# Optimization experiments

Measured on AMD Instinct MI355X. Metric: run time of the kernel, lower is better.

## Reference

```python
import jax, jax.numpy as jnp
import numpy as np

B, S, D, H = 2, 4096, 128, 128
EPS = 1e-6
NEG_INF = -1e30


def _complex_linear(xr, xi, Wr, Wi, br, bi):
    # x: (B,S,D); W: (H,D); complex linear (Wr + i Wi)(xr + i xi) + (br + i bi) per layer math:
    # real_out = (xr Wr + br) - (xi Wi + bi); imag_out = (xi Wr + br) + (xr Wi + bi)
    out_r = xr @ Wr.T + br - (xi @ Wi.T + bi)
    out_i = xi @ Wr.T + br + (xr @ Wi.T + bi)
    return out_r, out_i


def setup_inputs() -> dict:
    key = jax.random.key(0)
    ks = jax.random.split(key, 24)
    scale = 1.0 / np.sqrt(D)
    def W(k):
        return jax.random.normal(k, (H, D), jnp.float32) * scale
    def b(k):
        return jax.random.normal(k, (H,), jnp.float32) * 0.01
    inp = {
        "Z_q": jax.random.normal(ks[0], (B, 2, S, D, 1), jnp.float32),
        "Z_k": jax.random.normal(ks[1], (B, 2, S, D, 1), jnp.float32),
        "Z_v": jax.random.normal(ks[2], (B, 2, S, D, 1), jnp.float32),
        "Wq_r": W(ks[3]), "Wq_i": W(ks[4]), "bq_r": b(ks[5]), "bq_i": b(ks[6]),
        "Wk_r": W(ks[7]), "Wk_i": W(ks[8]), "bk_r": b(ks[9]), "bk_i": b(ks[10]),
        "Wv_r": W(ks[11]), "Wv_i": W(ks[12]), "bv_r": b(ks[13]), "bv_i": b(ks[14]),
        "Wp_r": W(ks[15]), "Wp_i": W(ks[16]), "bp_r": b(ks[17]), "bp_i": b(ks[18]),
        "noise_floor": jnp.asarray(1.0, jnp.float32),
        "tau": jnp.asarray(0.0, jnp.float32),
    }
    return inp


def reference(Z_q, Z_k, Z_v,
              Wq_r, Wq_i, bq_r, bq_i,
              Wk_r, Wk_i, bk_r, bk_i,
              Wv_r, Wv_i, bv_r, bv_i,
              Wp_r, Wp_i, bp_r, bp_i,
              noise_floor, tau):
    # squeeze trailing singleton; split real/imag -> (B,S,D)
    zqr, zqi = Z_q[:, 0, :, :, 0], Z_q[:, 1, :, :, 0]
    zkr, zki = Z_k[:, 0, :, :, 0], Z_k[:, 1, :, :, 0]
    zvr, zvi = Z_v[:, 0, :, :, 0], Z_v[:, 1, :, :, 0]

    Qr, Qi = _complex_linear(zqr, zqi, Wq_r, Wq_i, bq_r, bq_i)
    Kr, Ki = _complex_linear(zkr, zki, Wk_r, Wk_i, bk_r, bk_i)
    Vr, Vi = _complex_linear(zvr, zvi, Wv_r, Wv_i, bv_r, bv_i)

    # InverseMahalanobis: R2[b,i,j] = sum_h |Q[b,i]-K[b,j]|^2
    q2 = jnp.sum(Qr * Qr + Qi * Qi, axis=-1)          # (B,S)
    k2 = jnp.sum(Kr * Kr + Ki * Ki, axis=-1)          # (B,S)
    re_qk = (jnp.einsum('bsh,bth->bst', Qr, Kr)
             + jnp.einsum('bsh,bth->bst', Qi, Ki))    # (B,S,S)
    R2 = q2[:, :, None] + k2[:, None, :] - 2.0 * re_qk

    attn_scores = -jax.nn.softplus(tau) * jnp.log(noise_floor ** 2 + R2 + EPS)
    mask = jnp.tril(jnp.ones((S, S), dtype=bool))[None]
    attn_scores = jnp.where(mask, attn_scores, NEG_INF)
    attn_weights = jax.nn.softmax(attn_scores / jnp.sqrt(jnp.float32(H)), axis=-1)

    # attn (real) times complex V
    est_r = jnp.einsum('bst,bth->bsh', attn_weights, Vr)
    est_i = jnp.einsum('bst,bth->bsh', attn_weights, Vi)

    out_r, out_i = _complex_linear(est_r, est_i, Wp_r, Wp_i, bp_r, bp_i)
    out = jnp.stack((out_r, out_i), axis=1)[..., None]  # (B,2,S,H,1)
    return out, attn_weights
```

## Files before the change

### kernel.cpp

```cpp
#include <hip/hip_runtime.h>

#define S_LEN 4096
#define NBATCH 2
#define ROWS (NBATCH*S_LEN)
#define OUT_ELEMS 2097152

typedef _Float16 f16;
typedef _Float16 f16x8 __attribute__((ext_vector_type(8)));
typedef _Float16 f16x4 __attribute__((ext_vector_type(4)));
typedef float f32x4 __attribute__((ext_vector_type(4)));

#define MT_OFF    0x000000
#define BIAS_OFF  0x080000
#define SC_OFF    0x081000
#define QH_OFF    0x100000
#define KH_OFF    0x500000
#define VT_OFF    0x900000
#define Q2_OFF    0xD00000
#define K2_OFF    0xD10000
#define L_OFF     0xD20000
#define EST_OFF   0xE00000
#define PW_OFF    0x1600000
#define WS_NEED   0x5600000

#define MFMA16(A,B,C) __builtin_amdgcn_mfma_f32_16x16x32_f16(A,B,C,0,0,0)

__device__ __forceinline__ void async_cp16(f16* lds, const f16* g) {
  __builtin_amdgcn_global_load_lds(
      (const __attribute__((address_space(1))) void*)g,
      (__attribute__((address_space(3))) void*)lds, 16, 0, 0);
}

__device__ __forceinline__ void stage16(f16* lds, const f16* g, int stride, int tid) {
#pragma unroll
  for (int i = 0; i < 2; ++i) {
    int idx = i*256 + tid;
    int row = idx >> 2, c = idx & 3;
    async_cp16(lds + idx*8, g + (size_t)row*stride + c*8);
  }
}

__device__ __forceinline__ void stage32(f16* lds, const float* g, int stride, int tid,
                                        const float* rowscale) {
#pragma unroll
  for (int i = 0; i < 4; ++i) {
    int idx = i*256 + tid;
    int row = idx >> 3, c = idx & 7;
    const float4* gp = (const float4*)(g + (size_t)row*stride + c*4);
    float4 v = *gp;
    float sc = rowscale ? rowscale[row] : 1.0f;
    f16x4 h; h[0]=(f16)(v.x*sc); h[1]=(f16)(v.y*sc); h[2]=(f16)(v.z*sc); h[3]=(f16)(v.w*sc);
    *(f16x4*)(lds + row*32 + c*4) = h;
  }
}

__device__ __forceinline__ void mfma_step(const f16* Asm, const f16* Bsm, int lane,
                                          int wm, int wn, f32x4 acc[4][4]) {
  f16x8 a[4], b[4];
  int rr = lane & 15, kk = (lane >> 4) << 3;
#pragma unroll
  for (int i=0;i<4;i++) a[i] = *(const f16x8*)(Asm + (wm + i*16 + rr)*32 + kk);
#pragma unroll
  for (int j=0;j<4;j++) b[j] = *(const f16x8*)(Bsm + (wn + j*16 + rr)*32 + kk);
#pragma unroll
  for (int i=0;i<4;i++)
#pragma unroll
    for (int j=0;j<4;j++) acc[i][j] = MFMA16(a[i], b[j], acc[i][j]);
}

__global__ __launch_bounds__(256)
void k_build(const float* Wqr, const float* Wqi, const float* bqr, const float* bqi,
             const float* Wkr, const float* Wki, const float* bkr, const float* bki,
             const float* Wvr, const float* Wvi, const float* bvr, const float* bvi,
             const float* Wpr, const float* Wpi, const float* bpr, const float* bpi,
             f16* Mt, float* bias) {
  int mat = blockIdx.x;
  const float *Wr, *Wi, *br, *bi;
  if (mat == 0)      { Wr=Wqr; Wi=Wqi; br=bqr; bi=bqi; }
  else if (mat == 1) { Wr=Wkr; Wi=Wki; br=bkr; bi=bki; }
  else if (mat == 2) { Wr=Wvr; Wi=Wvi; br=bvr; bi=bvi; }
  else               { Wr=Wpr; Wi=Wpi; br=bpr; bi=bpi; }
  int idx = blockIdx.y*256 + threadIdx.x;
  int n = idx >> 8, k = idx & 255;
  int d = k & 127, h = n & 127;
  float w = (k < 128) ? ((n < 128) ? Wr[h*128+d] : Wi[h*128+d])
                      : ((n < 128) ? -Wi[h*128+d] : Wr[h*128+d]);
  Mt[mat*65536 + n*256 + k] = (f16)w;
  if (k == 0)
    bias[mat*256 + n] = (n < 128) ? (br[n] - bi[n]) : (br[n-128] + bi[n-128]);
}

__global__ __launch_bounds__(256)
void k_init(float* est, float* zreg, float* sc, const float* nf, const float* tau) {
  int idx = blockIdx.x*256 + threadIdx.x;
  if (idx < 524288) ((float4*)est)[idx] = make_float4(0.f,0.f,0.f,0.f);
  else { int j = idx - 524288; if (j < 12288) ((float4*)zreg)[j] = make_float4(0.f,0.f,0.f,0.f); }
  if (idx == 0) {
    float t = tau[0];
    float c = __builtin_log2f(1.0f + __builtin_exp2f(t * 1.4426950408889634f))
              * 0.6931471805599453f;
    sc[0] = -c * 0.08838834764831845f;
    sc[1] = nf[0]*nf[0] + 1e-6f;
  }
}

__global__ __launch_bounds__(256)
void k_proj(const float* Zq, const float* Zk, const float* Zv,
            const f16* Mt, const float* bias,
            f16* Qh, f16* Kh, f16* Vt, float* q2, float* k2) {
  __shared__ f16 Asm[128*32];
  __shared__ f16 Bsm[128*32];
  __shared__ float bias_s[128];
  int tid = threadIdx.x;
  int mode = blockIdx.z;
  int m0 = blockIdx.x * 128, n0 = blockIdx.y * 128;
  const float* Z = (mode==0) ? Zq : (mode==1 ? Zk : Zv);
  const f16* Bt = Mt + mode*65536;
  if (tid < 128) bias_s[tid] = bias[mode*256 + n0 + tid];
  int b = m0 >> 12, s0 = m0 & 4095;
  int lane = tid & 63, w = tid >> 6;
  int wm = (w >> 1)*64, wn = (w & 1)*64;
  f32x4 acc[4][4] = {};
  for (int kb = 0; kb < 8; ++kb) {
    int k0 = kb*32;
    int part = k0 >> 7, d0 = k0 & 127;
    const float* Ag = Z + (((size_t)(b*2 + part))*S_LEN + s0)*128 + d0;
    stage32(Asm, Ag, 128, tid, nullptr);
    stage16(Bsm, Bt + n0*256 + k0, 256, tid);
    __syncthreads();
    mfma_step(Asm, Bsm, lane, wm, wn, acc);
    __syncthreads();
  }
  int rr = (lane>>4)*4, cc = lane & 15;
  if (mode < 2) {
    f16* O = (mode==0) ? Qh : Kh;
    float rs[4][4];
#pragma unroll
    for (int i=0;i<4;i++)
#pragma unroll
      for (int r=0;r<4;r++) rs[i][r]=0.f;
#pragma unroll
    for (int i=0;i<4;i++)
#pragma unroll
      for (int j=0;j<4;j++) {
        int cl = wn + j*16 + cc;
        int cg = n0 + cl;
        float bv = bias_s[cl];
#pragma unroll
        for (int r=0;r<4;r++) {
          int rg = m0 + wm + i*16 + rr + r;
          f16 hv = (f16)(acc[i][j][r] + bv);
          O[(size_t)rg*256 + cg] = hv;
          float fv = (float)hv;
          rs[i][r] += fv*fv;
        }
      }
#pragma unroll
    for (int m=8;m>=1;m>>=1)
#pragma unroll
      for (int i=0;i<4;i++)
#pragma unroll
        for (int r=0;r<4;r++) rs[i][r] += __shfl_xor(rs[i][r], m, 64);
    if (cc == 0) {
      float* T = (mode==0) ? q2 : k2;
#pragma unroll
      for (int i=0;i<4;i++)
#pragma unroll
        for (int r=0;r<4;r++) {
          int rg = m0 + wm + i*16 + rr + r;
          atomicAdd(&T[rg], rs[i][r]);
        }
    }
  } else {
#pragma unroll
    for (int i=0;i<4;i++) {
      int t0 = s0 + wm + i*16 + rr;
#pragma unroll
      for (int j=0;j<4;j++) {
        int cl = wn + j*16 + cc;
        int cg = n0 + cl;
        float bv = bias_s[cl];
        f16x4 h4;
#pragma unroll
        for (int r=0;r<4;r++) h4[r] = (f16)(acc[i][j][r] + bv);
        *(f16x4*)(Vt + (size_t)b*1048576 + (size_t)cg*4096 + t0) = h4;
      }
    }
  }
}

__global__ __launch_bounds__(256)
void k_attn(const f16* Qh, const f16* Kh, const float* q2, const float* k2,
            const float* sc, float* lsum, f16* Pws, float* attn) {
  int x = blockIdx.x;
  int b = x >> 10, r = x & 1023;
  int sb = r >> 5, tb = r & 31;
  int s0 = sb*128, t0 = tb*128;
  int tid = threadIdx.x;
  if (tb > sb) {
    float4 z = make_float4(0.f,0.f,0.f,0.f);
    int row = tid >> 1, h = tid & 1;
    float4* p = (float4*)(attn + ((size_t)(b*S_LEN) + s0 + row)*S_LEN + t0 + h*64);
#pragma unroll
    for (int i=0;i<16;i++) p[i] = z;
    return;
  }
  __shared__ f16 Asm[128*32];
  __shared__ f16 Bsm[128*32];
  __shared__ float q2s[128], k2s[128];
  if (tid < 128) {
    q2s[tid] = q2[b*S_LEN + s0 + tid];
    k2s[tid] = k2[b*S_LEN + t0 + tid];
  }
  float kc = sc[0], nf2 = sc[1];
  int lane = tid & 63, w = tid >> 6;
  int wm = (w >> 1)*64, wn = (w & 1)*64;
  const f16* Ag = Qh + ((size_t)(b*S_LEN) + s0)*256;
  const f16* Bg = Kh + ((size_t)(b*S_LEN) + t0)*256;
  f32x4 acc[4][4] = {};
  for (int kb=0;kb<8;kb++) {
    stage16(Asm, Ag + kb*32, 256, tid);
    stage16(Bsm, Bg + kb*32, 256, tid);
    __syncthreads();
    mfma_step(Asm, Bsm, lane, wm, wn, acc);
    __syncthreads();
  }
  int rr = (lane>>4)*4, cc = lane & 15;
  bool diag = (tb == sb);
  float rs[4][4];
#pragma unroll
  for (int i=0;i<4;i++)
#pragma unroll
    for (int rg=0;rg<4;rg++) rs[i][rg]=0.f;
#pragma unroll
  for (int i=0;i<4;i++)
#pragma unroll
    for (int j=0;j<4;j++) {
      int cl = wn + j*16 + cc;
      float kv = k2s[cl];
#pragma unroll
      for (int rg=0;rg<4;rg++) {
        int rl = wm + i*16 + rr + rg;
        float xx = nf2 + q2s[rl] + kv - 2.0f*acc[i][j][rg];
        float P = __builtin_exp2f(kc * __builtin_log2f(__builtin_fmaxf(xx, 1e-6f)));
        if (diag && (t0+cl) > (s0+rl)) P = 0.f;
        Pws[((size_t)(b*S_LEN) + s0 + rl)*S_LEN + t0 + cl] = (f16)P;
        rs[i][rg] += P;
      }
    }
#pragma unroll
  for (int m=8;m>=1;m>>=1)
#pragma unroll
    for (int i=0;i<4;i++)
#pragma unroll
      for (int rg=0;rg<4;rg++) rs[i][rg] += __shfl_xor(rs[i][rg], m, 64);
  if (cc == 0)
#pragma unroll
    for (int i=0;i<4;i++)
#pragma unroll
      for (int rg=0;rg<4;rg++) {
        int rl = wm + i*16 + rr + rg;
        atomicAdd(&lsum[b*S_LEN + s0 + rl], rs[i][rg]);
      }
}

__global__ __launch_bounds__(256)
void k_pv(const f16* Pws, const f16* Vt, const float* lsum, float* est, float* attn) {
  __shared__ f16 Asm[128*32];
  __shared__ f16 Bsm[128*32];
  __shared__ float ls[128];
  int r = blockIdx.x;
  int nb = blockIdx.y, b = blockIdx.z;
  int sb = 0;
  while (r >= ((sb+4)>>2)) { r -= (sb+4)>>2; sb++; }
  int c = r;
  int s0 = sb*128, h0 = nb*128;
  int tid = threadIdx.x;
  bool wrb = (nb == 0);
  if (wrb && tid < 128) ls[tid] = 1.0f / lsum[b*S_LEN + s0 + tid];
  int lane = tid & 63, w = tid >> 6;
  int wm = (w>>1)*64, wn = (w&1)*64;
  int tb0 = c*4, tb1 = tb0 + 4; if (tb1 > sb+1) tb1 = sb+1;
  const f16* Abase = Pws + ((size_t)(b*S_LEN) + s0)*S_LEN;
  const f16* Bbase = Vt + (size_t)b*1048576 + (size_t)h0*4096;
  f32x4 acc[4][4] = {};
  int row2 = tid >> 1, half2 = tid & 1;
  for (int tb = tb0; tb < tb1; ++tb)
    for (int kk = 0; kk < 4; ++kk) {
      int t0 = tb*128 + kk*32;
      stage16(Asm, Abase + t0, S_LEN, tid);
      stage16(Bsm, Bbase + t0, 4096, tid);
      __syncthreads();
      if (wrb) {
        float invl = ls[row2];
        const f16x8* src = (const f16x8*)(Asm + row2*32 + half2*16);
        f16x8 v0 = src[0], v1 = src[1];
        float4* dst = (float4*)(attn + ((size_t)(b*S_LEN) + s0 + row2)*S_LEN + t0 + half2*16);
        float4 o;
        o.x=(float)v0[0]*invl; o.y=(float)v0[1]*invl; o.z=(float)v0[2]*invl; o.w=(float)v0[3]*invl; dst[0]=o;
        o.x=(float)v0[4]*invl; o.y=(float)v0[5]*invl; o.z=(float)v0[6]*invl; o.w=(float)v0[7]*invl; dst[1]=o;
        o.x=(float)v1[0]*invl; o.y=(float)v1[1]*invl; o.z=(float)v1[2]*invl; o.w=(float)v1[3]*invl; dst[2]=o;
        o.x=(float)v1[4]*invl; o.y=(float)v1[5]*invl; o.z=(float)v1[6]*invl; o.w=(float)v1[7]*invl; dst[3]=o;
      }
      mfma_step(Asm, Bsm, lane, wm, wn, acc);
      __syncthreads();
    }
  int rr = (lane>>4)*4, cc = lane & 15;
#pragma unroll
  for (int i=0;i<4;i++)
#pragma unroll
    for (int j=0;j<4;j++) {
      int cg = h0 + wn + j*16 + cc;
#pragma unroll
      for (int rg=0;rg<4;rg++) {
        int rgl = s0 + wm + i*16 + rr + rg;
        atomicAdd(&est[((size_t)(b*S_LEN) + rgl)*256 + cg], acc[i][j][rg]);
      }
    }
}

__global__ __launch_bounds__(256)
void k_out(const float* est, const f16* Mt, const float* bias, const float* lsum,
           float* outp) {
  __shared__ f16 Asm[128*32];
  __shared__ f16 Bsm[128*32];
  __shared__ float bias_s[128];
  __shared__ float ls[128];
  int m0 = blockIdx.x*128, n0 = blockIdx.y*128;
  int tid = threadIdx.x;
  int b = m0 >> 12, s0 = m0 & 4095;
  if (tid < 128) {
    bias_s[tid] = bias[3*256 + n0 + tid];
    ls[tid] = 1.0f / lsum[b*S_LEN + s0 + tid];
  }
  __syncthreads();
  int lane = tid & 63, w = tid >> 6;
  int wm = (w>>1)*64, wn = (w&1)*64;
  const f16* Bt = Mt + 3*65536;
  f32x4 acc[4][4] = {};
  for (int kb=0;kb<8;kb++) {
    stage32(Asm, est + (size_t)m0*256 + kb*32, 256, tid, ls);
    stage16(Bsm, Bt + n0*256 + kb*32, 256, tid);
    __syncthreads();
    mfma_step(Asm, Bsm, lane, wm, wn, acc);
    __syncthreads();
  }
  int rr = (lane>>4)*4, cc = lane & 15;
#pragma unroll
  for (int i=0;i<4;i++)
#pragma unroll
    for (int j=0;j<4;j++) {
      int cl = wn + j*16 + cc;
      int cg = n0 + cl;
      int comp = cg >> 7, h = cg & 127;
      float bv = bias_s[cl];
#pragma unroll
      for (int rg=0;rg<4;rg++) {
        int s = s0 + wm + i*16 + rr + rg;
        outp[(((size_t)(b*2 + comp))*S_LEN + s)*128 + h] = acc[i][j][rg] + bv;
      }
    }
}

extern "C" void kernel_launch(void* const* d_in, const int* in_sizes, int n_in,
                              void* d_out, int out_size, void* d_ws, size_t ws_size,
                              hipStream_t stream) {
  (void)in_sizes; (void)n_in; (void)out_size;
  if (ws_size < (size_t)WS_NEED) return;
  const float* Zq = (const float*)d_in[0];
  const float* Zk = (const float*)d_in[1];
  const float* Zv = (const float*)d_in[2];
  char* ws = (char*)d_ws;
  f16*   Mt   = (f16*)(ws + MT_OFF);
  float* bias = (float*)(ws + BIAS_OFF);
  float* sc   = (float*)(ws + SC_OFF);
  f16*   Qh   = (f16*)(ws + QH_OFF);
  f16*   Kh   = (f16*)(ws + KH_OFF);
  f16*   Vt   = (f16*)(ws + VT_OFF);
  float* q2   = (float*)(ws + Q2_OFF);
  float* k2   = (float*)(ws + K2_OFF);
  float* lsum = (float*)(ws + L_OFF);
  float* est  = (float*)(ws + EST_OFF);
  f16*   Pws  = (f16*)(ws + PW_OFF);
  float* outp = (float*)d_out;
  float* attn = outp + OUT_ELEMS;

  k_build<<<dim3(4,256), 256, 0, stream>>>(
      (const float*)d_in[3],  (const float*)d_in[4],  (const float*)d_in[5],  (const float*)d_in[6],
      (const float*)d_in[7],  (const float*)d_in[8],  (const float*)d_in[9],  (const float*)d_in[10],
      (const float*)d_in[11], (const float*)d_in[12], (const float*)d_in[13], (const float*)d_in[14],
      (const float*)d_in[15], (const float*)d_in[16], (const float*)d_in[17], (const float*)d_in[18],
      Mt, bias);
  k_init<<<2096, 256, 0, stream>>>(est, q2, sc, (const float*)d_in[19], (const float*)d_in[20]);
  k_proj<<<dim3(64,2,3), 256, 0, stream>>>(Zq, Zk, Zv, Mt, bias, Qh, Kh, Vt, q2, k2);
  k_attn<<<2048, 256, 0, stream>>>(Qh, Kh, q2, k2, sc, lsum, Pws, attn);
  k_pv<<<dim3(144,2,2), 256, 0, stream>>>(Pws, Vt, lsum, est, attn);
  k_out<<<dim3(64,2), 256, 0, stream>>>(est, Mt, bias, lsum, outp);
}
```

Before: 302.5 us.

## Fold output projection into V, double-buffer LDS, swizzle LDS layout

Precomputes V·Wp^T in a new kernel so the attention-times-V kernel accumulates final outputs directly via atomics into the output, which is pre-initialized with the bias, and removes the separate output projection kernel and the fp32 est buffer. It also double-buffers LDS staging in the projection, attention and PV kernels and XOR-swizzles the LDS layout to cut bank conflicts. The cost is an extra small GEMM and fp16 rounding of the projected V. The init kernel now writes the bias into the full output tensor.

New measurement: 318.2 us. 1.05x slower.

```diff
diff --git a/kernel.cpp b/kernel.cpp
--- a/kernel.cpp
+++ b/kernel.cpp
@@ -2,7 +2,6 @@
 
 #define S_LEN 4096
 #define NBATCH 2
-#define ROWS (NBATCH*S_LEN)
 #define OUT_ELEMS 2097152
 
 typedef _Float16 f16;
@@ -15,11 +14,11 @@
 #define SC_OFF    0x081000
 #define QH_OFF    0x100000
 #define KH_OFF    0x500000
-#define VT_OFF    0x900000
+#define VH_OFF    0x900000
 #define Q2_OFF    0xD00000
 #define K2_OFF    0xD10000
 #define L_OFF     0xD20000
-#define EST_OFF   0xE00000
+#define VPT_OFF   0xE00000
 #define PW_OFF    0x1600000
 #define WS_NEED   0x5600000
 
@@ -31,37 +30,39 @@
       (__attribute__((address_space(3))) void*)lds, 16, 0, 0);
 }
 
+
 __device__ __forceinline__ void stage16(f16* lds, const f16* g, int stride, int tid) {
 #pragma unroll
   for (int i = 0; i < 2; ++i) {
     int idx = i*256 + tid;
     int row = idx >> 2, c = idx & 3;
-    async_cp16(lds + idx*8, g + (size_t)row*stride + c*8);
-  }
-}
-
-__device__ __forceinline__ void stage32(f16* lds, const float* g, int stride, int tid,
-                                        const float* rowscale) {
+    int cs = c ^ ((row >> 1) & 3);
+    async_cp16(lds + idx*8, g + (size_t)row*stride + cs*8);
+  }
+}
+
+__device__ __forceinline__ void stage32(f16* lds, const float* g, int stride, int tid) {
 #pragma unroll
   for (int i = 0; i < 4; ++i) {
     int idx = i*256 + tid;
     int row = idx >> 3, c = idx & 7;
     const float4* gp = (const float4*)(g + (size_t)row*stride + c*4);
     float4 v = *gp;
-    float sc = rowscale ? rowscale[row] : 1.0f;
-    f16x4 h; h[0]=(f16)(v.x*sc); h[1]=(f16)(v.y*sc); h[2]=(f16)(v.z*sc); h[3]=(f16)(v.w*sc);
-    *(f16x4*)(lds + row*32 + c*4) = h;
+    f16x4 h; h[0]=(f16)v.x; h[1]=(f16)v.y; h[2]=(f16)v.z; h[3]=(f16)v.w;
+    int cl = (((c >> 1) ^ ((row >> 1) & 3)) << 1) | (c & 1);
+    *(f16x4*)(lds + row*32 + cl*4) = h;
   }
 }
 
 __device__ __forceinline__ void mfma_step(const f16* Asm, const f16* Bsm, int lane,
                                           int wm, int wn, f32x4 acc[4][4]) {
   f16x8 a[4], b[4];
-  int rr = lane & 15, kk = (lane >> 4) << 3;
-#pragma unroll
-  for (int i=0;i<4;i++) a[i] = *(const f16x8*)(Asm + (wm + i*16 + rr)*32 + kk);
-#pragma unroll
-  for (int j=0;j<4;j++) b[j] = *(const f16x8*)(Bsm + (wn + j*16 + rr)*32 + kk);
+  int rr = lane & 15;
+  int sc = (lane >> 4) ^ ((rr >> 1) & 3);
+#pragma unroll
+  for (int i=0;i<4;i++) a[i] = *(const f16x8*)(Asm + (wm + i*16 + rr)*32 + (sc<<3));
+#pragma unroll
+  for (int j=0;j<4;j++) b[j] = *(const f16x8*)(Bsm + (wn + j*16 + rr)*32 + (sc<<3));
 #pragma unroll
   for (int i=0;i<4;i++)
 #pragma unroll
@@ -91,10 +92,17 @@
 }
 
 __global__ __launch_bounds__(256)
-void k_init(float* est, float* zreg, float* sc, const float* nf, const float* tau) {
+void k_init(float* outp, float* zreg, float* sc, const float* bias,
+            const float* nf, const float* tau) {
   int idx = blockIdx.x*256 + threadIdx.x;
-  if (idx < 524288) ((float4*)est)[idx] = make_float4(0.f,0.f,0.f,0.f);
-  else { int j = idx - 524288; if (j < 12288) ((float4*)zreg)[j] = make_float4(0.f,0.f,0.f,0.f); }
+  if (idx < 1048576) {
+    int hq = idx & 31;
+    int comp = (idx >> 17) & 1;
+    ((float4*)outp)[idx] = *(const float4*)(bias + 3*256 + comp*128 + hq*4);
+  } else {
+    int j = idx - 1048576;
+    if (j < 12288) ((float4*)zreg)[j] = make_float4(0.f,0.f,0.f,0.f);
+  }
   if (idx == 0) {
     float t = tau[0];
     float c = __builtin_log2f(1.0f + __builtin_exp2f(t * 1.4426950408889634f))
@@ -107,9 +115,9 @@
 __global__ __launch_bounds__(256)
 void k_proj(const float* Zq, const float* Zk, const float* Zv,
             const f16* Mt, const float* bias,
-            f16* Qh, f16* Kh, f16* Vt, float* q2, float* k2) {
-  __shared__ f16 Asm[128*32];
-  __shared__ f16 Bsm[128*32];
+            f16* Qh, f16* Kh, f16* Vh, float* q2, float* k2) {
+  __shared__ f16 Asm[2][128*32];
+  __shared__ f16 Bsm[2][128*32];
   __shared__ float bias_s[128];
   int tid = threadIdx.x;
   int mode = blockIdx.z;
@@ -121,40 +129,48 @@
   int lane = tid & 63, w = tid >> 6;
   int wm = (w >> 1)*64, wn = (w & 1)*64;
   f32x4 acc[4][4] = {};
+  {
+    const float* Ag = Z + (((size_t)(b*2 + 0))*S_LEN + s0)*128 + 0;
+    stage32(Asm[0], Ag, 128, tid);
+    stage16(Bsm[0], Bt + n0*256 + 0, 256, tid);
+  }
+  __syncthreads();
   for (int kb = 0; kb < 8; ++kb) {
-    int k0 = kb*32;
-    int part = k0 >> 7, d0 = k0 & 127;
-    const float* Ag = Z + (((size_t)(b*2 + part))*S_LEN + s0)*128 + d0;
-    stage32(Asm, Ag, 128, tid, nullptr);
-    stage16(Bsm, Bt + n0*256 + k0, 256, tid);
+    int cur = kb & 1;
+    if (kb < 7) {
+      int k1 = (kb+1)*32;
+      int part = k1 >> 7, d0 = k1 & 127;
+      const float* Ag = Z + (((size_t)(b*2 + part))*S_LEN + s0)*128 + d0;
+      stage32(Asm[cur^1], Ag, 128, tid);
+      stage16(Bsm[cur^1], Bt + n0*256 + k1, 256, tid);
+    }
+    mfma_step(Asm[cur], Bsm[cur], lane, wm, wn, acc);
     __syncthreads();
-    mfma_step(Asm, Bsm, lane, wm, wn, acc);
-    __syncthreads();
   }
   int rr = (lane>>4)*4, cc = lane & 15;
+  f16* O = (mode==0) ? Qh : (mode==1 ? Kh : Vh);
+  float rs[4][4];
+#pragma unroll
+  for (int i=0;i<4;i++)
+#pragma unroll
+    for (int r=0;r<4;r++) rs[i][r]=0.f;
+#pragma unroll
+  for (int i=0;i<4;i++)
+#pragma unroll
+    for (int j=0;j<4;j++) {
+      int cl = wn + j*16 + cc;
+      int cg = n0 + cl;
+      float bv = bias_s[cl];
+#pragma unroll
+      for (int r=0;r<4;r++) {
+        int rg = m0 + wm + i*16 + rr + r;
+        f16 hv = (f16)(acc[i][j][r] + bv);
+        O[(size_t)rg*256 + cg] = hv;
+        float fv = (float)hv;
+        rs[i][r] += fv*fv;
+      }
+    }
   if (mode < 2) {
-    f16* O = (mode==0) ? Qh : Kh;
-    float rs[4][4];
-#pragma unroll
-    for (int i=0;i<4;i++)
-#pragma unroll
-      for (int r=0;r<4;r++) rs[i][r]=0.f;
-#pragma unroll
-    for (int i=0;i<4;i++)
-#pragma unroll
-      for (int j=0;j<4;j++) {
-        int cl = wn + j*16 + cc;
-        int cg = n0 + cl;
-        float bv = bias_s[cl];
-#pragma unroll
-        for (int r=0;r<4;r++) {
-          int rg = m0 + wm + i*16 + rr + r;
-          f16 hv = (f16)(acc[i][j][r] + bv);
-          O[(size_t)rg*256 + cg] = hv;
-          float fv = (float)hv;
-          rs[i][r] += fv*fv;
-        }
-      }
 #pragma unroll
     for (int m=8;m>=1;m>>=1)
 #pragma unroll
@@ -171,20 +187,42 @@
           atomicAdd(&T[rg], rs[i][r]);
         }
     }
-  } else {
-#pragma unroll
-    for (int i=0;i<4;i++) {
-      int t0 = s0 + wm + i*16 + rr;
-#pragma unroll
-      for (int j=0;j<4;j++) {
-        int cl = wn + j*16 + cc;
-        int cg = n0 + cl;
-        float bv = bias_s[cl];
-        f16x4 h4;
-#pragma unroll
-        for (int r=0;r<4;r++) h4[r] = (f16)(acc[i][j][r] + bv);
-        *(f16x4*)(Vt + (size_t)b*1048576 + (size_t)cg*4096 + t0) = h4;
-      }
+  }
+}
+
+__global__ __launch_bounds__(256)
+void k_vp(const f16* Vh, const f16* Mt, f16* VPt) {
+  __shared__ f16 Asm[2][128*32];
+  __shared__ f16 Bsm[2][128*32];
+  int t0 = blockIdx.x*128, n0 = blockIdx.y*128, b = blockIdx.z;
+  int tid = threadIdx.x;
+  int lane = tid & 63, w = tid >> 6;
+  int wm = (w>>1)*64, wn = (w&1)*64;
+  const f16* Ag = Mt + 3*65536 + n0*256;
+  const f16* Bg = Vh + ((size_t)(b*S_LEN) + t0)*256;
+  f32x4 acc[4][4] = {};
+  stage16(Asm[0], Ag, 256, tid);
+  stage16(Bsm[0], Bg, 256, tid);
+  __syncthreads();
+  for (int kb=0;kb<8;kb++) {
+    int cur = kb & 1;
+    if (kb < 7) {
+      stage16(Asm[cur^1], Ag + (kb+1)*32, 256, tid);
+      stage16(Bsm[cur^1], Bg + (kb+1)*32, 256, tid);
+    }
+    mfma_step(Asm[cur], Bsm[cur], lane, wm, wn, acc);
+    __syncthreads();
+  }
+  int rr = (lane>>4)*4, cc = lane & 15;
+#pragma unroll
+  for (int i=0;i<4;i++) {
+    int n = n0 + wm + i*16 + rr;
+#pragma unroll
+    for (int j=0;j<4;j++) {
+      int t = t0 + wn + j*16 + cc;
+#pragma unroll
+      for (int r=0;r<4;r++)
+        VPt[(size_t)b*1048576 + (size_t)(n + r)*4096 + t] = (f16)acc[i][j][r];
     }
   }
 }
@@ -205,8 +243,8 @@
     for (int i=0;i<16;i++) p[i] = z;
     return;
   }
-  __shared__ f16 Asm[128*32];
-  __shared__ f16 Bsm[128*32];
+  __shared__ f16 Asm[2][128*32];
+  __shared__ f16 Bsm[2][128*32];
   __shared__ float q2s[128], k2s[128];
   if (tid < 128) {
     q2s[tid] = q2[b*S_LEN + s0 + tid];
@@ -218,11 +256,16 @@
   const f16* Ag = Qh + ((size_t)(b*S_LEN) + s0)*256;
   const f16* Bg = Kh + ((size_t)(b*S_LEN) + t0)*256;
   f32x4 acc[4][4] = {};
+  stage16(Asm[0], Ag, 256, tid);
+  stage16(Bsm[0], Bg, 256, tid);
+  __syncthreads();
   for (int kb=0;kb<8;kb++) {
-    stage16(Asm, Ag + kb*32, 256, tid);
-    stage16(Bsm, Bg + kb*32, 256, tid);
-    __syncthreads();
-    mfma_step(Asm, Bsm, lane, wm, wn, acc);
+    int cur = kb & 1;
+    if (kb < 7) {
+      stage16(Asm[cur^1], Ag + (kb+1)*32, 256, tid);
+      stage16(Bsm[cur^1], Bg + (kb+1)*32, 256, tid);
+    }
+    mfma_step(Asm[cur], Bsm[cur], lane, wm, wn, acc);
     __syncthreads();
   }
   int rr = (lane>>4)*4, cc = lane & 15;
@@ -265,9 +308,9 @@
 }
 
 __global__ __launch_bounds__(256)
-void k_pv(const f16* Pws, const f16* Vt, const float* lsum, float* est, float* attn) {
-  __shared__ f16 Asm[128*32];
-  __shared__ f16 Bsm[128*32];
+void k_pv(const f16* Pws, const f16* VPt, const float* lsum, float* outp, float* attn) {
+  __shared__ f16 Asm[2][128*32];
+  __shared__ f16 Bsm[2][128*32];
   __shared__ float ls[128];
   int r = blockIdx.x;
   int nb = blockIdx.y, b = blockIdx.z;
@@ -277,87 +320,54 @@
   int s0 = sb*128, h0 = nb*128;
   int tid = threadIdx.x;
   bool wrb = (nb == 0);
-  if (wrb && tid < 128) ls[tid] = 1.0f / lsum[b*S_LEN + s0 + tid];
+  if (tid < 128) ls[tid] = 1.0f / lsum[b*S_LEN + s0 + tid];
   int lane = tid & 63, w = tid >> 6;
   int wm = (w>>1)*64, wn = (w&1)*64;
   int tb0 = c*4, tb1 = tb0 + 4; if (tb1 > sb+1) tb1 = sb+1;
-  const f16* Abase = Pws + ((size_t)(b*S_LEN) + s0)*S_LEN;
-  const f16* Bbase = Vt + (size_t)b*1048576 + (size_t)h0*4096;
+  int nt = (tb1 - tb0) * 4;
+  int base_t = tb0*128;
+  const f16* Abase = Pws + ((size_t)(b*S_LEN) + s0)*S_LEN + base_t;
+  const f16* Bbase = VPt + (size_t)b*1048576 + (size_t)h0*4096 + base_t;
   f32x4 acc[4][4] = {};
   int row2 = tid >> 1, half2 = tid & 1;
-  for (int tb = tb0; tb < tb1; ++tb)
-    for (int kk = 0; kk < 4; ++kk) {
-      int t0 = tb*128 + kk*32;
-      stage16(Asm, Abase + t0, S_LEN, tid);
-      stage16(Bsm, Bbase + t0, 4096, tid);
-      __syncthreads();
-      if (wrb) {
-        float invl = ls[row2];
-        const f16x8* src = (const f16x8*)(Asm + row2*32 + half2*16);
-        f16x8 v0 = src[0], v1 = src[1];
-        float4* dst = (float4*)(attn + ((size_t)(b*S_LEN) + s0 + row2)*S_LEN + t0 + half2*16);
-        float4 o;
-        o.x=(float)v0[0]*invl; o.y=(float)v0[1]*invl; o.z=(float)v0[2]*invl; o.w=(float)v0[3]*invl; dst[0]=o;
-        o.x=(float)v0[4]*invl; o.y=(float)v0[5]*invl; o.z=(float)v0[6]*invl; o.w=(float)v0[7]*invl; dst[1]=o;
-        o.x=(float)v1[0]*invl; o.y=(float)v1[1]*invl; o.z=(float)v1[2]*invl; o.w=(float)v1[3]*invl; dst[2]=o;
-        o.x=(float)v1[4]*invl; o.y=(float)v1[5]*invl; o.z=(float)v1[6]*invl; o.w=(float)v1[7]*invl; dst[3]=o;
-      }
-      mfma_step(Asm, Bsm, lane, wm, wn, acc);
-      __syncthreads();
-    }
+  int xs2 = (row2 >> 1) & 3;
+  stage16(Asm[0], Abase, S_LEN, tid);
+  stage16(Bsm[0], Bbase, 4096, tid);
+  __syncthreads();
+  for (int st = 0; st < nt; ++st) {
+    int cur = st & 1;
+    int t0 = base_t + st*32;
+    if (st + 1 < nt) {
+      stage16(Asm[cur^1], Abase + (st+1)*32, S_LEN, tid);
+      stage16(Bsm[cur^1], Bbase + (st+1)*32, 4096, tid);
+    }
+    if (wrb) {
+      float invl = ls[row2];
+      const f16* Arow = Asm[cur] + row2*32;
+      f16x8 v0 = *(const f16x8*)(Arow + (((2*half2  ) ^ xs2) << 3));
+      f16x8 v1 = *(const f16x8*)(Arow + (((2*half2+1) ^ xs2) << 3));
+      float4* dst = (float4*)(attn + ((size_t)(b*S_LEN) + s0 + row2)*S_LEN + t0 + half2*16);
+      float4 o;
+      o.x=(float)v0[0]*invl; o.y=(float)v0[1]*invl; o.z=(float)v0[2]*invl; o.w=(float)v0[3]*invl; dst[0]=o;
+      o.x=(float)v0[4]*invl; o.y=(float)v0[5]*invl; o.z=(float)v0[6]*invl; o.w=(float)v0[7]*invl; dst[1]=o;
+      o.x=(float)v1[0]*invl; o.y=(float)v1[1]*invl; o.z=(float)v1[2]*invl; o.w=(float)v1[3]*invl; dst[2]=o;
+      o.x=(float)v1[4]*invl; o.y=(float)v1[5]*invl; o.z=(float)v1[6]*invl; o.w=(float)v1[7]*invl; dst[3]=o;
+    }
+    mfma_step(Asm[cur], Bsm[cur], lane, wm, wn, acc);
+    __syncthreads();
+  }
   int rr = (lane>>4)*4, cc = lane & 15;
 #pragma unroll
   for (int i=0;i<4;i++)
 #pragma unroll
     for (int j=0;j<4;j++) {
       int cg = h0 + wn + j*16 + cc;
+      int comp = cg >> 7, h = cg & 127;
 #pragma unroll
       for (int rg=0;rg<4;rg++) {
-        int rgl = s0 + wm + i*16 + rr + rg;
-        atomicAdd(&est[((size_t)(b*S_LEN) + rgl)*256 + cg], acc[i][j][rg]);
-      }
-    }
-}
-
-__global__ __launch_bounds__(256)
-void k_out(const float* est, const f16* Mt, const float* bias, const float* lsum,
-           float* outp) {
-  __shared__ f16 Asm[128*32];
-  __shared__ f16 Bsm[128*32];
-  __shared__ float bias_s[128];
-  __shared__ float ls[128];
-  int m0 = blockIdx.x*128, n0 = blockIdx.y*128;
-  int tid = threadIdx.x;
-  int b = m0 >> 12, s0 = m0 & 4095;
-  if (tid < 128) {
-    bias_s[tid] = bias[3*256 + n0 + tid];
-    ls[tid] = 1.0f / lsum[b*S_LEN + s0 + tid];
-  }
-  __syncthreads();
-  int lane = tid & 63, w = tid >> 6;
-  int wm = (w>>1)*64, wn = (w&1)*64;
-  const f16* Bt = Mt + 3*65536;
-  f32x4 acc[4][4] = {};
-  for (int kb=0;kb<8;kb++) {
-    stage32(Asm, est + (size_t)m0*256 + kb*32, 256, tid, ls);
-    stage16(Bsm, Bt + n0*256 + kb*32, 256, tid);
-    __syncthreads();
-    mfma_step(Asm, Bsm, lane, wm, wn, acc);
-    __syncthreads();
-  }
-  int rr = (lane>>4)*4, cc = lane & 15;
-#pragma unroll
-  for (int i=0;i<4;i++)
-#pragma unroll
-    for (int j=0;j<4;j++) {
-      int cl = wn + j*16 + cc;
-      int cg = n0 + cl;
-      int comp = cg >> 7, h = cg & 127;
-      float bv = bias_s[cl];
-#pragma unroll
-      for (int rg=0;rg<4;rg++) {
-        int s = s0 + wm + i*16 + rr + rg;
-        outp[(((size_t)(b*2 + comp))*S_LEN + s)*128 + h] = acc[i][j][rg] + bv;
+        int rl = wm + i*16 + rr + rg;
+        float v = acc[i][j][rg] * ls[rl];
+        atomicAdd(&outp[(((size_t)(b*2 + comp))*S_LEN + s0 + rl)*128 + h], v);
       }
     }
 }
@@ -376,11 +386,11 @@
   float* sc   = (float*)(ws + SC_OFF);
   f16*   Qh   = (f16*)(ws + QH_OFF);
   f16*   Kh   = (f16*)(ws + KH_OFF);
-  f16*   Vt   = (f16*)(ws + VT_OFF);
+  f16*   Vh   = (f16*)(ws + VH_OFF);
   float* q2   = (float*)(ws + Q2_OFF);
   float* k2   = (float*)(ws + K2_OFF);
   float* lsum = (float*)(ws + L_OFF);
-  float* est  = (float*)(ws + EST_OFF);
+  f16*   VPt  = (f16*)(ws + VPT_OFF);
   f16*   Pws  = (f16*)(ws + PW_OFF);
   float* outp = (float*)d_out;
   float* attn = outp + OUT_ELEMS;
@@ -391,9 +401,9 @@
       (const float*)d_in[11], (const float*)d_in[12], (const float*)d_in[13], (const float*)d_in[14],
       (const float*)d_in[15], (const float*)d_in[16], (const float*)d_in[17], (const float*)d_in[18],
       Mt, bias);
-  k_init<<<2096, 256, 0, stream>>>(est, q2, sc, (const float*)d_in[19], (const float*)d_in[20]);
-  k_proj<<<dim3(64,2,3), 256, 0, stream>>>(Zq, Zk, Zv, Mt, bias, Qh, Kh, Vt, q2, k2);
+  k_init<<<4144, 256, 0, stream>>>(outp, q2, sc, bias, (const float*)d_in[19], (const float*)d_in[20]);
+  k_proj<<<dim3(64,2,3), 256, 0, stream>>>(Zq, Zk, Zv, Mt, bias, Qh, Kh, Vh, q2, k2);
+  k_vp<<<dim3(32,2,2), 256, 0, stream>>>(Vh, Mt, VPt);
   k_attn<<<2048, 256, 0, stream>>>(Qh, Kh, q2, k2, sc, lsum, Pws, attn);
-  k_pv<<<dim3(144,2,2), 256, 0, stream>>>(Pws, Vt, lsum, est, attn);
-  k_out<<<dim3(64,2), 256, 0, stream>>>(est, Mt, bias, lsum, outp);
-}
+  k_pv<<<dim3(144,2,2), 256, 0, stream>>>(Pws, VPt, lsum, outp, attn);
+}
```
